# Kernel tuning notes

Hardware: AMD Instinct MI355X
Metric: run time of the kernel (lower is better)

Reference implementation:

```python
import jax, jax.numpy as jnp
import numpy as np

B, T, M, D = 4, 512, 16, 128
P, H = 128, 4
E = P // H


def _glorot(k, shape, fan_in, fan_out):
    lim = np.sqrt(6.0 / (fan_in + fan_out)).astype(np.float32)
    return jax.random.uniform(k, shape, jnp.float32, -lim, lim)


def setup_inputs() -> dict:
    key = jax.random.key(0)
    ks = jax.random.split(key, 12)
    inp = jax.random.normal(ks[0], (B, T, M, D), jnp.float32)
    pos = jax.random.normal(ks[1], (B, T, 1, D), jnp.float32)
    # padding mask: valid time steps per batch element (ensures no fully-masked softmax row)
    lengths = jax.random.randint(ks[2], (B,), T // 2, T + 1)
    mask = jnp.broadcast_to(jnp.arange(T)[None, :, None] < lengths[:, None, None], (B, T, M))
    Wq = _glorot(ks[3], (M, P, D), D, P)
    Wk = _glorot(ks[4], (M, P, D), D, P)
    Wv = _glorot(ks[5], (M, P, D), D, P)
    Wq_t = _glorot(ks[6], (M, P, D), D, P)
    Wk_t = _glorot(ks[7], (M, P, D), D, P)
    Bq = jnp.zeros((M, P), jnp.float32)
    Bk = jnp.zeros((M, P), jnp.float32)
    Bv = jnp.zeros((M, P), jnp.float32)
    Bq_t = jnp.zeros((M, P), jnp.float32)
    Bk_t = jnp.zeros((M, P), jnp.float32)
    return {"inp": inp, "pos": pos, "mask": mask,
            "Wq": Wq, "Bq": Bq, "Wk": Wk, "Bk": Bk, "Wv": Wv, "Bv": Bv,
            "Wq_t": Wq_t, "Bq_t": Bq_t, "Wk_t": Wk_t, "Bk_t": Bk_t}


def reference(inp, pos, mask, Wq, Bq, Wk, Bk, Wv, Bv, Wq_t, Bq_t, Wk_t, Bk_t):
    b, t, m, d = inp.shape
    p = Wq.shape[1]
    h, e = H, P // H
    # per-modality projections: (m,p,d) x (b,t,m,d) -> (b,t,m,p)
    q = jnp.einsum('mpd,btmd->btmp', Wq, inp) + Bq
    k = jnp.einsum('mpd,btmd->btmp', Wk, inp) + Bk
    v = jnp.einsum('mpd,btmd->btmp', Wv, inp) + Bv
    pos0 = pos[:, :, 0, :]  # (b,t,d); broadcasts across m
    q_t = jnp.einsum('mpd,btd->btmp', Wq_t, pos0) + Bq_t
    k_t = jnp.einsum('mpd,btd->btmp', Wk_t, pos0) + Bk_t

    def split_heads(x):  # (b,t,m,p) -> (b,m,h,t,e)
        return x.reshape(b, t, m, h, e).transpose(0, 2, 3, 1, 4)

    q, k, v, q_t, k_t = map(split_heads, (q, k, v, q_t, k_t))
    # dual bilinear score: content + positional
    score = (jnp.einsum('bmhte,bmhse->bmhts', q, k)
             + jnp.einsum('bmhte,bmhse->bmhts', q_t, k_t)) / (2.0 * np.sqrt(e).astype(np.float32))
    causal = jnp.tril(jnp.ones((t, t), bool))  # (t,t)
    score = jnp.where(causal, score, -jnp.inf)
    km = mask.transpose(0, 2, 1)[:, :, None, None, :]  # (b,m,1,1,t)
    score = jnp.where(km, score, -jnp.inf)
    w = jax.nn.softmax(score, axis=-1)
    w = jnp.where(km, w, 0.0)
    w = jnp.where(causal, w, 0.0)
    # dropout is identity at inference (drop_rate ignored)
    out = jnp.einsum('bmhts,bmhse->bmhte', w, v)
    return out.transpose(0, 3, 1, 2, 4).reshape(b, t, m, p)
```

## Files before the change

### kernel.cpp

```cpp
#include <hip/hip_runtime.h>

#define Bn 4
#define Tn 512
#define Mn 16
#define Dn 128
#define Pn 128
#define Hn 4
#define SCALE 0.08838834764831845f

typedef unsigned short u16;
typedef unsigned int u32;
typedef short s16;
typedef __attribute__((ext_vector_type(8))) s16 bf16x8;
typedef __attribute__((ext_vector_type(4))) float f32x4;

__device__ __forceinline__ u16 f2b(float f) {
  u32 x; __builtin_memcpy(&x, &f, 4);
  x += 0x7fffu + ((x >> 16) & 1u);
  return (u16)(x >> 16);
}
__device__ __forceinline__ u32 pack2(float a, float b) {
  return (u32)f2b(a) | ((u32)f2b(b) << 16);
}
__device__ __forceinline__ bf16x8 ld8(const u16* p) {
  bf16x8 r; __builtin_memcpy(&r, p, 16); return r;
}
__device__ __forceinline__ bf16x8 cvt8(float4 lo, float4 hi) {
  uint4 dd;
  dd.x = pack2(lo.x, lo.y); dd.y = pack2(lo.z, lo.w);
  dd.z = pack2(hi.x, hi.y); dd.w = pack2(hi.z, hi.w);
  bf16x8 r; __builtin_memcpy(&r, &dd, 16); return r;
}
__device__ __forceinline__ f32x4 mfma16(bf16x8 a, bf16x8 b, f32x4 c) {
  return __builtin_amdgcn_mfma_f32_16x16x32_bf16(a, b, c, 0, 0, 0);
}

__global__ __launch_bounds__(256, 2) void proj_v3(
    const float* __restrict__ inp, const float* __restrict__ pos,
    const float* __restrict__ Wq, const float* __restrict__ Wk,
    const float* __restrict__ Wv, const float* __restrict__ Wqt,
    const float* __restrict__ Wkt,
    const float* __restrict__ Bq, const float* __restrict__ Bk,
    const float* __restrict__ Bv, const float* __restrict__ Bqt,
    const float* __restrict__ Bkt,
    u16* __restrict__ Qa, u16* __restrict__ Ka, u16* __restrict__ Qb,
    u16* __restrict__ Kb, u16* __restrict__ Vt) {
  __shared__ __align__(16) u16 Xs[128 * 136];
  __shared__ __align__(16) u16 Ws[128 * 136];

  const int tid = threadIdx.x;
  const int bid = blockIdx.x;
  const bool isA = bid < 256;
  const int sub = bid & 255;
  const int m = sub & 15;
  const int rt0 = (sub >> 4) * 128;

  const int wv = tid >> 6, lane = tid & 63;
  const int quad = lane >> 4, l16 = lane & 15;

  const size_t wofs = (size_t)m * Pn * Dn;
  const float* W0 = (isA ? Wq : Wqt) + wofs;
  const float* W1 = (isA ? Wk : Wkt) + wofs;
  const float* Bb0 = isA ? Bq : Bqt;
  const float* Bb1 = isA ? Bk : Bkt;
  u16* dst0 = isA ? Qa : Qb;
  u16* dst1 = isA ? Ka : Kb;

#pragma unroll
  for (int it = 0; it < 16; ++it) {
    const int c = tid + it * 256;
    const int row = c >> 5, col4 = (c & 31) * 4;
    const size_t sx = isA ? (((size_t)(rt0 + row) * Mn + m) * Dn + col4)
                          : ((size_t)(rt0 + row) * Dn + col4);
    const float4 x = *(const float4*)((isA ? inp : pos) + sx);
    ushort4 h; h.x = f2b(x.x); h.y = f2b(x.y); h.z = f2b(x.z); h.w = f2b(x.w);
    *(ushort4*)&Xs[row * 136 + col4] = h;
  }
  if (isA) {
#pragma unroll
    for (int it = 0; it < 16; ++it) {
      const int c = tid + it * 256;
      const int row = c >> 5, col4 = (c & 31) * 4;
      const float4 w = *(const float4*)(Wv + wofs + (size_t)row * Dn + col4);
      ushort4 h; h.x = f2b(w.x); h.y = f2b(w.y); h.z = f2b(w.z); h.w = f2b(w.w);
      *(ushort4*)&Ws[row * 136 + col4] = h;
    }
  }

  float4 raw[16];
#pragma unroll
  for (int pf = 0; pf < 2; ++pf)
#pragma unroll
    for (int kc2 = 0; kc2 < 4; ++kc2) {
      const float* p = W0 + (size_t)(wv * 32 + pf * 16 + l16) * Dn + kc2 * 32 + quad * 8;
      raw[(pf * 4 + kc2) * 2] = *(const float4*)p;
      raw[(pf * 4 + kc2) * 2 + 1] = *(const float4*)(p + 4);
    }

  __syncthreads();

  const int b = rt0 >> 9;
  const int tb = rt0 & (Tn - 1);

  if (isA) {
    f32x4 acc[2][8];
#pragma unroll
    for (int i = 0; i < 2; ++i)
#pragma unroll
      for (int n = 0; n < 8; ++n) acc[i][n] = (f32x4){0.f, 0.f, 0.f, 0.f};
#pragma unroll
    for (int kc2 = 0; kc2 < 4; ++kc2) {
      const int xo = kc2 * 32 + quad * 8;
      const bf16x8 a0 = ld8(&Xs[(wv * 32 + l16) * 136 + xo]);
      const bf16x8 a1 = ld8(&Xs[(wv * 32 + 16 + l16) * 136 + xo]);
#pragma unroll
      for (int n = 0; n < 8; ++n) {
        const bf16x8 bn = ld8(&Ws[(n * 16 + l16) * 136 + xo]);
        acc[0][n] = mfma16(a0, bn, acc[0][n]);
        acc[1][n] = mfma16(a1, bn, acc[1][n]);
      }
    }
    const int tl0 = tb + wv * 32;
#pragma unroll
    for (int n = 0; n < 8; ++n) {
      const int h = n >> 1, e = (n & 1) * 16 + l16;
      const float bias = Bv[m * Pn + n * 16 + l16];
      const int bmh = (b * Mn + m) * Hn + h;
      const size_t rowv = ((size_t)bmh * 32 + e) * Tn;
#pragma unroll
      for (int qs = 0; qs < 2; ++qs) {
        const int t0 = tl0 + qs * 16 + quad * 4;
        uint2 d;
        d.x = pack2(acc[qs][n][0] + bias, acc[qs][n][1] + bias);
        d.y = pack2(acc[qs][n][2] + bias, acc[qs][n][3] + bias);
        *(uint2*)&Vt[rowv + t0] = d;
      }
    }
  }

  const int bmh = (b * Mn + m) * Hn + wv;

  bf16x8 frag[2][4];
#pragma unroll
  for (int pf = 0; pf < 2; ++pf)
#pragma unroll
    for (int kc2 = 0; kc2 < 4; ++kc2)
      frag[pf][kc2] = cvt8(raw[(pf * 4 + kc2) * 2], raw[(pf * 4 + kc2) * 2 + 1]);
#pragma unroll
  for (int pf = 0; pf < 2; ++pf)
#pragma unroll
    for (int kc2 = 0; kc2 < 4; ++kc2) {
      const float* p = W1 + (size_t)(wv * 32 + pf * 16 + l16) * Dn + kc2 * 32 + quad * 8;
      raw[(pf * 4 + kc2) * 2] = *(const float4*)p;
      raw[(pf * 4 + kc2) * 2 + 1] = *(const float4*)(p + 4);
    }

#pragma unroll
  for (int ts = 0; ts < 2; ++ts) {
    f32x4 acc[2][8];
#pragma unroll
    for (int i = 0; i < 2; ++i)
#pragma unroll
      for (int n = 0; n < 8; ++n) acc[i][n] = (f32x4){0.f, 0.f, 0.f, 0.f};
#pragma unroll
    for (int kc2 = 0; kc2 < 4; ++kc2) {
      const int xo = kc2 * 32 + quad * 8;
      const bf16x8 a0 = frag[0][kc2];
      const bf16x8 a1 = frag[1][kc2];
#pragma unroll
      for (int n = 0; n < 8; ++n) {
        const bf16x8 bn = ld8(&Xs[(n * 16 + l16) * 136 + xo]);
        acc[0][n] = mfma16(a0, bn, acc[0][n]);
        acc[1][n] = mfma16(a1, bn, acc[1][n]);
      }
    }
    if (ts == 0) {
#pragma unroll
      for (int pf = 0; pf < 2; ++pf)
#pragma unroll
        for (int kc2 = 0; kc2 < 4; ++kc2)
          frag[pf][kc2] = cvt8(raw[(pf * 4 + kc2) * 2], raw[(pf * 4 + kc2) * 2 + 1]);
    }
    const float* Bb = ts ? Bb1 : Bb0;
    u16* dst = ts ? dst1 : dst0;
#pragma unroll
    for (int pf = 0; pf < 2; ++pf) {
      const int p0 = wv * 32 + pf * 16 + quad * 4;
      const float4 b4 = *(const float4*)&Bb[m * Pn + p0];
#pragma unroll
      for (int tf = 0; tf < 8; ++tf) {
        const int t = tb + tf * 16 + l16;
        float v0 = acc[pf][tf][0] + b4.x;
        float v1 = acc[pf][tf][1] + b4.y;
        float v2 = acc[pf][tf][2] + b4.z;
        float v3 = acc[pf][tf][3] + b4.w;
        if (ts == 0) { v0 *= SCALE; v1 *= SCALE; v2 *= SCALE; v3 *= SCALE; }
        uint2 d; d.x = pack2(v0, v1); d.y = pack2(v2, v3);
        *(uint2*)&dst[((size_t)bmh * Tn + t) * 32 + pf * 16 + quad * 4] = d;
      }
    }
  }
}

__global__ __launch_bounds__(256, 4) void attn_flash(
    const void* __restrict__ mask,
    const u16* __restrict__ Qa, const u16* __restrict__ Ka,
    const u16* __restrict__ Qb, const u16* __restrict__ Kb,
    const u16* __restrict__ Vt, float* __restrict__ out) {
  __shared__ __align__(16) u16 Ps[4 * 32 * 72];

  const int tid = threadIdx.x;
  const int blk = blockIdx.x;
  const int wv = tid >> 6, lane = tid & 63;
  const int quad = lane >> 4, l16 = lane & 15;

  const int bmh = blk & 255;
  const int qt = wv * 4 + (blk >> 8);
  const int b = bmh >> 6;

  const u32 w0 = ((const u32*)mask)[0];
  const int mode = (w0 == 1u) ? 0 : (w0 == 0x3F800000u) ? 1
                 : (w0 == 0x3F803F80u) ? 2 : 3;
  int c = 0;
  for (int t = lane; t < Tn; t += 64) {
    const size_t idx = ((size_t)b * Tn + t) * Mn;
    int nz;
    if (mode == 0)      nz = (((const int*)mask)[idx] != 0);
    else if (mode == 1) nz = (((const u32*)mask)[idx] != 0u);
    else if (mode == 2) nz = (((const u16*)mask)[idx] != 0);
    else                nz = (((const unsigned char*)mask)[idx] != 0);
    c += nz;
  }
  c += __shfl_xor(c, 1);  c += __shfl_xor(c, 2);  c += __shfl_xor(c, 4);
  c += __shfl_xor(c, 8);  c += __shfl_xor(c, 16); c += __shfl_xor(c, 32);
  const int len = c;

  const int q0 = qt * 32;
  const size_t rowbase = (size_t)bmh * Tn;
  const size_t vbase = (size_t)bmh * 32 * Tn;
  u16* myPs = &Ps[wv * 32 * 72];
  const int mm = (bmh >> 2) & (Mn - 1);
  const int h = bmh & (Hn - 1);

  bf16x8 qf[2][2];
#pragma unroll
  for (int qs = 0; qs < 2; ++qs) {
    const size_t r = (rowbase + q0 + qs * 16 + l16) * 32 + quad * 8;
    qf[qs][0] = ld8(Qa + r);
    qf[qs][1] = ld8(Qb + r);
  }

  f32x4 O[2][2];
#pragma unroll
  for (int qs = 0; qs < 2; ++qs)
#pragma unroll
    for (int es = 0; es < 2; ++es) O[qs][es] = (f32x4){0.f, 0.f, 0.f, 0.f};
  float mrow[2] = {-1e30f, -1e30f}, lsum[2] = {0.f, 0.f};

  const int s_hi = min(q0 + 32, len);
  for (int s0 = 0; s0 < s_hi; s0 += 64) {
    f32x4 S[2][4];
    __builtin_amdgcn_s_setprio(1);
#pragma unroll
    for (int st = 0; st < 4; ++st) {
      const size_t kr = (rowbase + s0 + st * 16 + l16) * 32 + quad * 8;
      const bf16x8 k0 = ld8(Ka + kr);
      const bf16x8 k1 = ld8(Kb + kr);
#pragma unroll
      for (int qs = 0; qs < 2; ++qs)
        S[qs][st] = mfma16(k1, qf[qs][1],
                           mfma16(k0, qf[qs][0], (f32x4){0.f, 0.f, 0.f, 0.f}));
    }
    __builtin_amdgcn_s_setprio(0);

#pragma unroll
    for (int qs = 0; qs < 2; ++qs) {
      const int q = q0 + qs * 16 + l16;
      const int qcap = min(q, len - 1);
      const int sb = s0 + quad * 4;
      float cmax = -1e30f;
#pragma unroll
      for (int st = 0; st < 4; ++st)
#pragma unroll
        for (int reg = 0; reg < 4; ++reg) {
          const int s = sb + st * 16 + reg;
          const float v = (s <= qcap) ? S[qs][st][reg] : -1e30f;
          S[qs][st][reg] = v;
          cmax = fmaxf(cmax, v);
        }
      cmax = fmaxf(cmax, __shfl_xor(cmax, 16));
      cmax = fmaxf(cmax, __shfl_xor(cmax, 32));
      const float mnew = fmaxf(mrow[qs], cmax);
      const float alpha = __expf(mrow[qs] - mnew);
      mrow[qs] = mnew;
      float rsum = 0.f;
      u32 pk[4][2];
#pragma unroll
      for (int st = 0; st < 4; ++st) {
        const float p0 = __expf(S[qs][st][0] - mnew);
        const float p1 = __expf(S[qs][st][1] - mnew);
        const float p2 = __expf(S[qs][st][2] - mnew);
        const float p3 = __expf(S[qs][st][3] - mnew);
        rsum += (p0 + p1) + (p2 + p3);
        pk[st][0] = pack2(p0, p1);
        pk[st][1] = pack2(p2, p3);
      }
      rsum += __shfl_xor(rsum, 16);
      rsum += __shfl_xor(rsum, 32);
      lsum[qs] = lsum[qs] * alpha + rsum;
#pragma unroll
      for (int es = 0; es < 2; ++es)
#pragma unroll
        for (int reg = 0; reg < 4; ++reg) O[qs][es][reg] *= alpha;
#pragma unroll
      for (int st = 0; st < 4; ++st) {
        uint2 d; d.x = pk[st][0]; d.y = pk[st][1];
        *(uint2*)&myPs[(qs * 16 + l16) * 72 + st * 16 + quad * 4] = d;
      }
    }

    __builtin_amdgcn_s_setprio(1);
#pragma unroll
    for (int kc = 0; kc < 2; ++kc) {
      const int ko = kc * 32 + quad * 8;
      const bf16x8 pf0 = ld8(&myPs[l16 * 72 + ko]);
      const bf16x8 pf1 = ld8(&myPs[(16 + l16) * 72 + ko]);
      const bf16x8 vf0 = ld8(Vt + vbase + (size_t)l16 * Tn + s0 + ko);
      const bf16x8 vf1 = ld8(Vt + vbase + (size_t)(16 + l16) * Tn + s0 + ko);
      O[0][0] = mfma16(vf0, pf0, O[0][0]);
      O[0][1] = mfma16(vf1, pf0, O[0][1]);
      O[1][0] = mfma16(vf0, pf1, O[1][0]);
      O[1][1] = mfma16(vf1, pf1, O[1][1]);
    }
    __builtin_amdgcn_s_setprio(0);
  }

#pragma unroll
  for (int qs = 0; qs < 2; ++qs) {
    const float linv = 1.0f / lsum[qs];
    const int t = q0 + qs * 16 + l16;
    const size_t ob = (((size_t)b * Tn + t) * Mn + mm) * Pn + h * 32 + quad * 4;
#pragma unroll
    for (int es = 0; es < 2; ++es) {
      float4 o;
      o.x = O[qs][es][0] * linv; o.y = O[qs][es][1] * linv;
      o.z = O[qs][es][2] * linv; o.w = O[qs][es][3] * linv;
      *(float4*)&out[ob + es * 16] = o;
    }
  }
}

extern "C" void kernel_launch(void* const* d_in, const int* in_sizes, int n_in,
                              void* d_out, int out_size, void* d_ws, size_t ws_size,
                              hipStream_t stream) {
  const float* inp = (const float*)d_in[0];
  const float* pos = (const float*)d_in[1];
  const void* mask = d_in[2];
  const float* Wq  = (const float*)d_in[3];
  const float* Bq  = (const float*)d_in[4];
  const float* Wk  = (const float*)d_in[5];
  const float* Bk  = (const float*)d_in[6];
  const float* Wv  = (const float*)d_in[7];
  const float* Bv  = (const float*)d_in[8];
  const float* Wqt = (const float*)d_in[9];
  const float* Bqt = (const float*)d_in[10];
  const float* Wkt = (const float*)d_in[11];
  const float* Bkt = (const float*)d_in[12];
  float* out = (float*)d_out;

  const size_t nA = (size_t)Bn * Mn * Hn * Tn * 32;
  u16* Qa = (u16*)d_ws;
  u16* Ka = Qa + nA;
  u16* Qb = Ka + nA;
  u16* Kb = Qb + nA;
  u16* Vt = Kb + nA;

  proj_v3<<<512, 256, 0, stream>>>(
      inp, pos, Wq, Wk, Wv, Wqt, Wkt, Bq, Bk, Bv, Bqt, Bkt,
      Qa, Ka, Qb, Kb, Vt);
  attn_flash<<<1024, 256, 0, stream>>>(mask, Qa, Ka, Qb, Kb, Vt, out);
}
```

Baseline: 139.3 us.

## Split attention KV loop across wave pairs with shared-memory softmax merge

```diff
diff --git a/kernel.cpp b/kernel.cpp
--- a/kernel.cpp
+++ b/kernel.cpp
@@ -7,6 +7,7 @@
 #define Pn 128
 #define Hn 4
 #define SCALE 0.08838834764831845f
+#define NEGBIG -3e38f
 
 typedef unsigned short u16;
 typedef unsigned int u32;
@@ -139,7 +140,6 @@
   }
 
   const int bmh = (b * Mn + m) * Hn + wv;
-
   bf16x8 frag[2][4];
 #pragma unroll
   for (int pf = 0; pf < 2; ++pf)
@@ -202,7 +202,7 @@
   }
 }
 
-__global__ __launch_bounds__(256, 4) void attn_flash(
+__global__ __launch_bounds__(256, 4) void attn_sk(
     const void* __restrict__ mask,
     const u16* __restrict__ Qa, const u16* __restrict__ Ka,
     const u16* __restrict__ Qb, const u16* __restrict__ Kb,
@@ -210,13 +210,16 @@
   __shared__ __align__(16) u16 Ps[4 * 32 * 72];
 
   const int tid = threadIdx.x;
-  const int blk = blockIdx.x;
   const int wv = tid >> 6, lane = tid & 63;
   const int quad = lane >> 4, l16 = lane & 15;
 
-  const int bmh = blk & 255;
-  const int qt = wv * 4 + (blk >> 8);
+  const int unit = blockIdx.x * 2 + (wv >> 1);
+  const int sub = wv & 1;
+  const int bmh = unit & 255;
+  const int qt = unit >> 8;
   const int b = bmh >> 6;
+  const int mm = (bmh >> 2) & (Mn - 1);
+  const int h = bmh & (Hn - 1);
 
   const u32 w0 = ((const u32*)mask)[0];
   const int mode = (w0 == 1u) ? 0 : (w0 == 0x3F800000u) ? 1
@@ -236,11 +239,11 @@
   const int len = c;
 
   const int q0 = qt * 32;
+  const int s_hi = min(q0 + 32, len);
+  const int NC = (s_hi + 63) >> 6;
   const size_t rowbase = (size_t)bmh * Tn;
   const size_t vbase = (size_t)bmh * 32 * Tn;
   u16* myPs = &Ps[wv * 32 * 72];
-  const int mm = (bmh >> 2) & (Mn - 1);
-  const int h = bmh & (Hn - 1);
 
   bf16x8 qf[2][2];
 #pragma unroll
@@ -257,8 +260,8 @@
     for (int es = 0; es < 2; ++es) O[qs][es] = (f32x4){0.f, 0.f, 0.f, 0.f};
   float mrow[2] = {-1e30f, -1e30f}, lsum[2] = {0.f, 0.f};
 
-  const int s_hi = min(q0 + 32, len);
-  for (int s0 = 0; s0 < s_hi; s0 += 64) {
+  for (int ci = sub; ci < NC; ci += 2) {
+    const int s0 = ci << 6;
     f32x4 S[2][4];
     __builtin_amdgcn_s_setprio(1);
 #pragma unroll
@@ -278,13 +281,13 @@
       const int q = q0 + qs * 16 + l16;
       const int qcap = min(q, len - 1);
       const int sb = s0 + quad * 4;
-      float cmax = -1e30f;
+      float cmax = NEGBIG;
 #pragma unroll
       for (int st = 0; st < 4; ++st)
 #pragma unroll
         for (int reg = 0; reg < 4; ++reg) {
           const int s = sb + st * 16 + reg;
-          const float v = (s <= qcap) ? S[qs][st][reg] : -1e30f;
+          const float v = (s <= qcap) ? S[qs][st][reg] : NEGBIG;
           S[qs][st][reg] = v;
           cmax = fmaxf(cmax, v);
         }
@@ -335,17 +338,41 @@
     __builtin_amdgcn_s_setprio(0);
   }
 
-#pragma unroll
-  for (int qs = 0; qs < 2; ++qs) {
-    const float linv = 1.0f / lsum[qs];
-    const int t = q0 + qs * 16 + l16;
-    const size_t ob = (((size_t)b * Tn + t) * Mn + mm) * Pn + h * 32 + quad * 4;
-#pragma unroll
-    for (int es = 0; es < 2; ++es) {
-      float4 o;
-      o.x = O[qs][es][0] * linv; o.y = O[qs][es][1] * linv;
-      o.z = O[qs][es][2] * linv; o.w = O[qs][es][3] * linv;
-      *(float4*)&out[ob + es * 16] = o;
+  float* mslab = (float*)&Ps[(wv & ~1) * 32 * 72];
+  if (sub == 0) {
+#pragma unroll
+    for (int qs = 0; qs < 2; ++qs) {
+      const int rowf = (qs * 16 + l16) * 34;
+#pragma unroll
+      for (int es = 0; es < 2; ++es)
+#pragma unroll
+        for (int reg = 0; reg < 4; ++reg)
+          mslab[rowf + es * 16 + quad * 4 + reg] = O[qs][es][reg];
+      if (quad == 0) { mslab[rowf + 32] = mrow[qs]; mslab[rowf + 33] = lsum[qs]; }
+    }
+  }
+  __syncthreads();
+  if (sub == 1) {
+#pragma unroll
+    for (int qs = 0; qs < 2; ++qs) {
+      const int rowf = (qs * 16 + l16) * 34;
+      const float mA = mslab[rowf + 32], lA = mslab[rowf + 33];
+      const float mM = fmaxf(mA, mrow[qs]);
+      const float aA = __expf(mA - mM);
+      const float aB = __expf(mrow[qs] - mM);
+      const float lM = lA * aA + lsum[qs] * aB;
+      const float linv = 1.0f / lM;
+      const int t = q0 + qs * 16 + l16;
+      const size_t ob = (((size_t)b * Tn + t) * Mn + mm) * Pn + h * 32 + quad * 4;
+#pragma unroll
+      for (int es = 0; es < 2; ++es) {
+        float4 o;
+        o.x = (mslab[rowf + es * 16 + quad * 4 + 0] * aA + O[qs][es][0] * aB) * linv;
+        o.y = (mslab[rowf + es * 16 + quad * 4 + 1] * aA + O[qs][es][1] * aB) * linv;
+        o.z = (mslab[rowf + es * 16 + quad * 4 + 2] * aA + O[qs][es][2] * aB) * linv;
+        o.w = (mslab[rowf + es * 16 + quad * 4 + 3] * aA + O[qs][es][3] * aB) * linv;
+        *(float4*)&out[ob + es * 16] = o;
+      }
     }
   }
 }
@@ -378,5 +405,5 @@
   proj_v3<<<512, 256, 0, stream>>>(
       inp, pos, Wq, Wk, Wv, Wqt, Wkt, Bq, Bk, Bv, Bqt, Bkt,
       Qa, Ka, Qb, Kb, Vt);
-  attn_flash<<<1024, 256, 0, stream>>>(mask, Qa, Ka, Qb, Kb, Vt, out);
-}
+  attn_sk<<<2048, 256, 0, stream>>>(mask, Qa, Ka, Qb, Kb, Vt, out);
+}
```

Result: slower. 143.6 us (+3.0%).
